# Kernel optimization log

Hardware: AMD Instinct MI355X
Metric: run time of the kernel (lower is better)

The kernel has to match this reference:

```python
import jax, jax.numpy as jnp
import numpy as np

DIM, DK, DV = 1024, 128, 128

def setup_inputs() -> dict:
    key = jax.random.key(0)
    ks = jax.random.split(key, 7)
    X = jax.random.normal(ks[0], (4, 4096, DIM), dtype=jnp.float32)
    s = DIM ** -0.5
    Wq = jax.random.normal(ks[1], (DIM, DK), dtype=jnp.float32) * s
    bq = jnp.zeros((DK,), dtype=jnp.float32)
    Wk = jax.random.normal(ks[2], (DIM, DK), dtype=jnp.float32) * s
    bk = jnp.zeros((DK,), dtype=jnp.float32)
    Wv = jax.random.normal(ks[3], (DIM, DV), dtype=jnp.float32) * s
    bv = jnp.zeros((DV,), dtype=jnp.float32)
    return {"X": X, "Wq": Wq, "bq": bq, "Wk": Wk, "bk": bk, "Wv": Wv, "bv": bv}

def reference(X, Wq, bq, Wk, bk, Wv, bv):
    scale = DK ** -0.5
    q = X @ Wq + bq              # [B, S, dk]
    k = X @ Wk + bk              # [B, S, dk]
    v = X @ Wv + bv              # [B, S, dv]
    attn = jnp.einsum('bqd,bkd->bqk', q, k) * scale  # [B, S, S]
    attn = jax.nn.softmax(attn, axis=-1)
    return jnp.einsum('bqk,bkd->bqd', attn, v)       # [B, S, dv]
```

## Files before the change

### kernel.cpp

```cpp
#include <hip/hip_runtime.h>

#define NB 4
#define SEQ 4096
#define DIMK 1024
#define DKV 128
#define SCALE 0.08838834764831845f

typedef float  f32x4  __attribute__((ext_vector_type(4)));
typedef float  f32x16 __attribute__((ext_vector_type(16)));
typedef _Float16 f16x8 __attribute__((ext_vector_type(8)));

static __device__ __forceinline__ int pkrtz(float a, float b) {
    auto h = __builtin_amdgcn_cvt_pkrtz(a, b);
    return __builtin_bit_cast(int, h);
}

static __device__ __forceinline__ void gll16(const void* g, void* l) {
    __builtin_amdgcn_global_load_lds((const __attribute__((address_space(1))) char*)g,
                                     (__attribute__((address_space(3))) char*)l, 16, 0, 0);
}

__global__ void prep_wt(const float* __restrict__ Wq, const float* __restrict__ Wk,
                        const float* __restrict__ Wv, _Float16* __restrict__ WT) {
    int tid = blockIdx.x * 256 + threadIdx.x;
    int n  = tid & 127;
    int k  = (tid >> 7) & 1023;
    int w3 = tid >> 17;
    const float* W = (w3 == 0) ? Wq : (w3 == 1) ? Wk : Wv;
    WT[((size_t)w3 * 128 + n) * 1024 + k] = (_Float16)W[(size_t)k * 128 + n];
}

__global__ __launch_bounds__(256, 2) void qkv_proj(
    const float* __restrict__ X,
    const float* __restrict__ bq, const float* __restrict__ bk, const float* __restrict__ bv,
    const _Float16* __restrict__ WT,
    _Float16* __restrict__ Qh, _Float16* __restrict__ Kh, _Float16* __restrict__ VTh) {

    __shared__ __attribute__((aligned(16))) char WTs[2][128 * 144];
    const int t = threadIdx.x;
    const int w = t >> 6, l = t & 63;
    const int lrow = l & 15, lg = l >> 4;
    const int w3   = blockIdx.x % 3;
    const int tile = blockIdx.x / 3;
    const int r0 = tile * 64;

    f32x4 acc[8] = {};
    const float* xrow = X + (size_t)(r0 + w * 16 + lrow) * DIMK;
    const _Float16* Wbase = WT + (size_t)w3 * 128 * 1024;

    const int srow = t >> 3, spart = t & 7;

    {
        int4 wreg[4];
        #pragma unroll
        for (int i = 0; i < 4; ++i)
            wreg[i] = *(const int4*)(Wbase + (size_t)(srow + 32 * i) * 1024 + spart * 8);
        #pragma unroll
        for (int i = 0; i < 4; ++i)
            *(int4*)(WTs[0] + (srow + 32 * i) * 144 + spart * 16) = wreg[i];
    }
    float4 xc0 = *(const float4*)(xrow + lg * 8);
    float4 xc1 = *(const float4*)(xrow + lg * 8 + 4);
    float4 xc2 = *(const float4*)(xrow + 32 + lg * 8);
    float4 xc3 = *(const float4*)(xrow + 32 + lg * 8 + 4);
    __syncthreads();

    for (int kt = 0; kt < 16; ++kt) {
        const int cur = kt & 1;
        const int k0n = ((kt + 1) & 15) * 64;
        float4 xn0 = *(const float4*)(xrow + k0n + lg * 8);
        float4 xn1 = *(const float4*)(xrow + k0n + lg * 8 + 4);
        float4 xn2 = *(const float4*)(xrow + k0n + 32 + lg * 8);
        float4 xn3 = *(const float4*)(xrow + k0n + 32 + lg * 8 + 4);
        int4 wreg[4];
        #pragma unroll
        for (int i = 0; i < 4; ++i)
            wreg[i] = *(const int4*)(Wbase + (size_t)(srow + 32 * i) * 1024 + k0n + spart * 8);

        #pragma unroll
        for (int kk = 0; kk < 2; ++kk) {
            f16x8 a;
            float4 u = kk ? xc2 : xc0, v = kk ? xc3 : xc1;
            a[0] = (_Float16)u.x; a[1] = (_Float16)u.y; a[2] = (_Float16)u.z; a[3] = (_Float16)u.w;
            a[4] = (_Float16)v.x; a[5] = (_Float16)v.y; a[6] = (_Float16)v.z; a[7] = (_Float16)v.w;
            #pragma unroll
            for (int n = 0; n < 8; ++n) {
                f16x8 bf = *(const f16x8*)(WTs[cur] + (n * 16 + lrow) * 144 +
                                           kk * 64 + lg * 16);
                acc[n] = __builtin_amdgcn_mfma_f32_16x16x32_f16(a, bf, acc[n], 0, 0, 0);
            }
        }
        #pragma unroll
        for (int i = 0; i < 4; ++i)
            *(int4*)(WTs[cur ^ 1] + (srow + 32 * i) * 144 + spart * 16) = wreg[i];
        __syncthreads();
        xc0 = xn0; xc1 = xn1; xc2 = xn2; xc3 = xn3;
    }

    const float* bias = (w3 == 0) ? bq : (w3 == 1) ? bk : bv;
    #pragma unroll
    for (int n = 0; n < 8; ++n) {
        int col = n * 16 + lrow;
        float bv_ = bias[col];
        #pragma unroll
        for (int j = 0; j < 4; ++j) {
            int grow = r0 + w * 16 + lg * 4 + j;
            float val = acc[n][j] + bv_;
            if (w3 == 0) {
                Qh[(size_t)grow * DKV + col] = (_Float16)(val * SCALE);
            } else if (w3 == 1) {
                Kh[(size_t)grow * DKV + col] = (_Float16)val;
            } else {
                int b = grow >> 12, sp = grow & 4095;
                VTh[((size_t)b * DKV + col) * SEQ + sp] = (_Float16)val;
            }
        }
    }
}

__global__ __launch_bounds__(256, 2) void attn_kernel(
    const _Float16* __restrict__ Qh, const _Float16* __restrict__ Kh,
    const _Float16* __restrict__ VTh, float* __restrict__ out) {

    __shared__ __attribute__((aligned(16))) char lds[65536];

    const int t = threadIdx.x;
    const int w = t >> 6, l = t & 63;
    const int lq = l & 31;
    const int hi = l >> 5;

    const int work = (blockIdx.x & 7) * 64 + (blockIdx.x >> 3);
    const int b  = work >> 7;
    const int qt = work & 127;
    const int q0 = qt * 32;

    char* Kw = lds + w * 16384;
    char* Vw = Kw + 8192;

    f16x8 qf[8];
    #pragma unroll
    for (int c = 0; c < 8; ++c)
        qf[c] = *(const f16x8*)(Qh + (size_t)(b * SEQ + q0 + lq) * DKV + c * 16 + hi * 8);

    f32x16 o[4] = {};
    float m = -INFINITY, lsum = 0.f;

    const _Float16* Kbase = Kh + (size_t)(b * SEQ + w * 1024) * DKV;
    const _Float16* Vbase = VTh + (size_t)b * DKV * SEQ + w * 1024;

    const int krow_ = l >> 4;
    const int vdv_  = l >> 2;

#define STAGE_K(KOFF) {                                                                   \
        _Pragma("unroll")                                                                 \
        for (int i = 0; i < 8; ++i) {                                                     \
            int row = 4 * i + krow_;                                                      \
            int part = (l & 15) ^ (row & 15);                                             \
            gll16(Kbase + (size_t)((KOFF) + row) * DKV + part * 8, Kw + i * 1024);        \
        }                                                                                 \
    }
#define STAGE_V(KOFF) {                                                                   \
        _Pragma("unroll")                                                                 \
        for (int i = 0; i < 8; ++i) {                                                     \
            int dv = 16 * i + vdv_;                                                       \
            int p = (l & 3) ^ ((dv >> 1) & 3);                                            \
            gll16(Vbase + (size_t)dv * SEQ + (KOFF) + p * 8, Vw + i * 1024);              \
        }                                                                                 \
    }

    STAGE_K(0)
    STAGE_V(0)

    for (int kt = 0; kt < 32; ++kt) {
        const int kn = ((kt + 1) & 31) * 32;

        asm volatile("s_waitcnt vmcnt(0)" ::: "memory");
        __builtin_amdgcn_sched_barrier(0);

        f32x16 sa = {}, sb = {};
        #pragma unroll
        for (int c = 0; c < 4; ++c) {
            f16x8 kfa = *(const f16x8*)(Kw + lq * 256 +
                                        (((2 * c + hi) * 16) ^ ((lq & 15) << 4)));
            f16x8 kfb = *(const f16x8*)(Kw + lq * 256 +
                                        (((2 * (c + 4) + hi) * 16) ^ ((lq & 15) << 4)));
            sa = __builtin_amdgcn_mfma_f32_32x32x16_f16(kfa, qf[c], sa, 0, 0, 0);
            sb = __builtin_amdgcn_mfma_f32_32x32x16_f16(kfb, qf[c + 4], sb, 0, 0, 0);
        }
        f32x16 s = sa + sb;

        asm volatile("s_waitcnt lgkmcnt(0)" ::: "memory");
        __builtin_amdgcn_sched_barrier(0);
        STAGE_K(kn)

        float red[8];
        #pragma unroll
        for (int r = 0; r < 8; ++r) red[r] = fmaxf(s[2 * r], s[2 * r + 1]);
        #pragma unroll
        for (int r = 0; r < 4; ++r) red[r] = fmaxf(red[r], red[r + 4]);
        red[0] = fmaxf(red[0], red[2]);
        red[1] = fmaxf(red[1], red[3]);
        float tm = fmaxf(red[0], red[1]);
        tm = fmaxf(tm, __shfl_xor(tm, 32));

        if (__any(tm > m + 8.f)) {
            float mnew = fmaxf(m, tm);
            float corr = __expf(m - mnew);
            m = mnew;
            lsum *= corr;
            #pragma unroll
            for (int dvt = 0; dvt < 4; ++dvt) o[dvt] *= corr;
        }
        #pragma unroll
        for (int r = 0; r < 16; ++r) s[r] = __expf(s[r] - m);
        float sr[8];
        #pragma unroll
        for (int r = 0; r < 8; ++r) sr[r] = s[2 * r] + s[2 * r + 1];
        #pragma unroll
        for (int r = 0; r < 4; ++r) sr[r] += sr[r + 4];
        sr[0] += sr[2]; sr[1] += sr[3];
        float ts = sr[0] + sr[1];
        ts += __shfl_xor(ts, 32);
        lsum += ts;

        int wv[8];
        #pragma unroll
        for (int i = 0; i < 8; ++i) wv[i] = pkrtz(s[2 * i], s[2 * i + 1]);

        #pragma unroll
        for (int s_ = 0; s_ < 2; ++s_) {
            const int base = s_ * 4;
            int x0 = __shfl_xor(wv[base + 0], 32);
            int x1 = __shfl_xor(wv[base + 1], 32);
            int x2 = __shfl_xor(wv[base + 2], 32);
            int x3 = __shfl_xor(wv[base + 3], 32);
            union { int i[4]; f16x8 v; } bu;
            bu.i[0] = hi ? x2 : wv[base + 0];
            bu.i[1] = hi ? x3 : wv[base + 1];
            bu.i[2] = hi ? wv[base + 2] : x0;
            bu.i[3] = hi ? wv[base + 3] : x1;
            #pragma unroll
            for (int dvt = 0; dvt < 4; ++dvt) {
                int rv = dvt * 32 + lq;
                f16x8 vf = *(const f16x8*)(Vw + rv * 64 +
                                           (((s_ * 2 + hi) ^ ((rv >> 1) & 3)) * 16));
                o[dvt] = __builtin_amdgcn_mfma_f32_32x32x16_f16(vf, bu.v, o[dvt], 0, 0, 0);
            }
        }

        asm volatile("s_waitcnt lgkmcnt(0)" ::: "memory");
        __builtin_amdgcn_sched_barrier(0);
        STAGE_V(kn)
    }
#undef STAGE_K
#undef STAGE_V

    float* obuf  = (float*)lds;
    float* mlbuf = (float*)(lds + 49152);

    __syncthreads();
    if (w == 1 || w == 3) {
        int sb_ = (w == 3);
        #pragma unroll
        for (int dvt = 0; dvt < 4; ++dvt)
            #pragma unroll
            for (int r = 0; r < 16; ++r)
                obuf[sb_ * 4096 + (dvt * 16 + r) * 64 + l] = o[dvt][r];
        if (l < 32) {
            mlbuf[sb_ * 64 + l * 2 + 0] = m;
            mlbuf[sb_ * 64 + l * 2 + 1] = lsum;
        }
    }
    __syncthreads();
    if (w == 0 || w == 2) {
        int sb_ = (w == 2);
        float mo  = mlbuf[sb_ * 64 + lq * 2 + 0];
        float lo_ = mlbuf[sb_ * 64 + lq * 2 + 1];
        float mn = fmaxf(m, mo);
        float ca = __expf(m - mn);
        float cb = __expf(mo - mn);
        m = mn;
        lsum = lsum * ca + lo_ * cb;
        #pragma unroll
        for (int dvt = 0; dvt < 4; ++dvt)
            #pragma unroll
            for (int r = 0; r < 16; ++r)
                o[dvt][r] = o[dvt][r] * ca + obuf[sb_ * 4096 + (dvt * 16 + r) * 64 + l] * cb;
    }
    __syncthreads();
    if (w == 2) {
        #pragma unroll
        for (int dvt = 0; dvt < 4; ++dvt)
            #pragma unroll
            for (int r = 0; r < 16; ++r)
                obuf[(dvt * 16 + r) * 64 + l] = o[dvt][r];
        if (l < 32) {
            mlbuf[l * 2 + 0] = m;
            mlbuf[l * 2 + 1] = lsum;
        }
    }
    __syncthreads();
    if (w == 0) {
        float mo  = mlbuf[lq * 2 + 0];
        float lo_ = mlbuf[lq * 2 + 1];
        float mn = fmaxf(m, mo);
        float ca = __expf(m - mn);
        float cb = __expf(mo - mn);
        float rl = 1.0f / (lsum * ca + lo_ * cb);
        #pragma unroll
        for (int dvt = 0; dvt < 4; ++dvt)
            #pragma unroll
            for (int r = 0; r < 16; ++r)
                o[dvt][r] = (o[dvt][r] * ca + obuf[(dvt * 16 + r) * 64 + l] * cb) * rl;
    }
    __syncthreads();
    float* tbuf = (float*)lds;
    if (w == 0) {
        #pragma unroll
        for (int dvt = 0; dvt < 4; ++dvt)
            #pragma unroll
            for (int r = 0; r < 16; ++r) {
                int dv = dvt * 32 + (r & 3) + 8 * (r >> 2) + 4 * hi;
                tbuf[lq * 132 + dv] = o[dvt][r];
            }
    }
    __syncthreads();
    const size_t obase = (size_t)(b * SEQ + qt * 32) * DKV;
    int row = t >> 3, c0 = (t & 7) * 16;
    #pragma unroll
    for (int i = 0; i < 4; ++i) {
        float4 v = *(const float4*)(tbuf + row * 132 + c0 + i * 4);
        *(float4*)(out + obase + row * 128 + c0 + i * 4) = v;
    }
}

extern "C" void kernel_launch(void* const* d_in, const int* in_sizes, int n_in,
                              void* d_out, int out_size, void* d_ws, size_t ws_size,
                              hipStream_t stream) {
    const float* X  = (const float*)d_in[0];
    const float* Wq = (const float*)d_in[1];
    const float* bq = (const float*)d_in[2];
    const float* Wk = (const float*)d_in[3];
    const float* bk = (const float*)d_in[4];
    const float* Wv = (const float*)d_in[5];
    const float* bv = (const float*)d_in[6];
    float* out = (float*)d_out;

    const size_t nqe = (size_t)NB * SEQ * DKV;
    _Float16* Qh  = (_Float16*)d_ws;
    _Float16* Kh  = Qh  + nqe;
    _Float16* VTh = Kh  + nqe;
    _Float16* WTh = VTh + nqe;

    prep_wt<<<(3 * 1024 * 128) / 256, 256, 0, stream>>>(Wq, Wk, Wv, WTh);
    qkv_proj<<<(NB * SEQ / 64) * 3, 256, 0, stream>>>(X, bq, bk, bv, WTh, Qh, Kh, VTh);
    attn_kernel<<<NB * 128, 256, 0, stream>>>(Qh, Kh, VTh, out);
}
```

Baseline: 118.9 us.

## Split attention keys across two blocks with combine kernel and shared K/V LDS buffer

Splits the key range into two halves when workspace allows, so the attention grid doubles from 512 to 1024 blocks. The second split writes fp16 partial outputs plus per-row max and sum, and a new combine kernel merges the two splits into the output. K and V now share one per-wave LDS buffer, halving LDS to about 33KB so more blocks fit per CU, with the K and V stages serialized inside each iteration. The qkv_proj block order is also remapped. The cost is an extra kernel, extra global traffic, fp16 rounding of half the partial outputs, and less load/compute overlap because of the shared buffer.

```diff
diff --git a/kernel.cpp b/kernel.cpp
--- a/kernel.cpp
+++ b/kernel.cpp
@@ -4,11 +4,13 @@
 #define SEQ 4096
 #define DIMK 1024
 #define DKV 128
+#define NS (NB * SEQ)
 #define SCALE 0.08838834764831845f
 
 typedef float  f32x4  __attribute__((ext_vector_type(4)));
 typedef float  f32x16 __attribute__((ext_vector_type(16)));
 typedef _Float16 f16x8 __attribute__((ext_vector_type(8)));
+typedef _Float16 f16x4 __attribute__((ext_vector_type(4)));
 
 static __device__ __forceinline__ int pkrtz(float a, float b) {
     auto h = __builtin_amdgcn_cvt_pkrtz(a, b);
@@ -40,8 +42,9 @@
     const int t = threadIdx.x;
     const int w = t >> 6, l = t & 63;
     const int lrow = l & 15, lg = l >> 4;
-    const int w3   = blockIdx.x % 3;
-    const int tile = blockIdx.x / 3;
+    const int work = (blockIdx.x & 7) * 96 + (blockIdx.x >> 3);
+    const int w3   = work % 3;
+    const int tile = work / 3;
     const int r0 = tile * 64;
 
     f32x4 acc[8] = {};
@@ -120,22 +123,26 @@
 
 __global__ __launch_bounds__(256, 2) void attn_kernel(
     const _Float16* __restrict__ Qh, const _Float16* __restrict__ Kh,
-    const _Float16* __restrict__ VTh, float* __restrict__ out) {
-
-    __shared__ __attribute__((aligned(16))) char lds[65536];
+    const _Float16* __restrict__ VTh, float* __restrict__ out,
+    _Float16* __restrict__ O1h, float* __restrict__ ml,
+    int nsplit, int kps) {
+
+    __shared__ __attribute__((aligned(16))) char lds[33280];
 
     const int t = threadIdx.x;
     const int w = t >> 6, l = t & 63;
     const int lq = l & 31;
     const int hi = l >> 5;
 
-    const int work = (blockIdx.x & 7) * 64 + (blockIdx.x >> 3);
-    const int b  = work >> 7;
+    const int cpx = gridDim.x >> 3;
+    const int work = (blockIdx.x & 7) * cpx + (blockIdx.x >> 3);
+    const int bs = work >> 7;
     const int qt = work & 127;
+    const int b  = (nsplit == 2) ? (bs >> 1) : bs;
+    const int s  = (nsplit == 2) ? (bs & 1) : 0;
     const int q0 = qt * 32;
 
-    char* Kw = lds + w * 16384;
-    char* Vw = Kw + 8192;
+    char* KVw = lds + w * 8192;
 
     f16x8 qf[8];
     #pragma unroll
@@ -145,8 +152,11 @@
     f32x16 o[4] = {};
     float m = -INFINITY, lsum = 0.f;
 
-    const _Float16* Kbase = Kh + (size_t)(b * SEQ + w * 1024) * DKV;
-    const _Float16* Vbase = VTh + (size_t)b * DKV * SEQ + w * 1024;
+    const int wkeys = kps >> 2;
+    const int kts = wkeys >> 5;
+    const int koff0 = s * kps + w * wkeys;
+    const _Float16* Kbase = Kh + (size_t)(b * SEQ + koff0) * DKV;
+    const _Float16* Vbase = VTh + (size_t)b * DKV * SEQ + koff0;
 
     const int krow_ = l >> 4;
     const int vdv_  = l >> 2;
@@ -156,7 +166,7 @@
         for (int i = 0; i < 8; ++i) {                                                     \
             int row = 4 * i + krow_;                                                      \
             int part = (l & 15) ^ (row & 15);                                             \
-            gll16(Kbase + (size_t)((KOFF) + row) * DKV + part * 8, Kw + i * 1024);        \
+            gll16(Kbase + (size_t)((KOFF) + row) * DKV + part * 8, KVw + i * 1024);       \
         }                                                                                 \
     }
 #define STAGE_V(KOFF) {                                                                   \
@@ -164,15 +174,15 @@
         for (int i = 0; i < 8; ++i) {                                                     \
             int dv = 16 * i + vdv_;                                                       \
             int p = (l & 3) ^ ((dv >> 1) & 3);                                            \
-            gll16(Vbase + (size_t)dv * SEQ + (KOFF) + p * 8, Vw + i * 1024);              \
+            gll16(Vbase + (size_t)dv * SEQ + (KOFF) + p * 8, KVw + i * 1024);             \
         }                                                                                 \
     }
 
     STAGE_K(0)
-    STAGE_V(0)
-
-    for (int kt = 0; kt < 32; ++kt) {
-        const int kn = ((kt + 1) & 31) * 32;
+
+    for (int kt = 0; kt < kts; ++kt) {
+        const int k0 = kt * 32;
+        const int knext = (kt + 1 == kts) ? 0 : (kt + 1) * 32;
 
         asm volatile("s_waitcnt vmcnt(0)" ::: "memory");
         __builtin_amdgcn_sched_barrier(0);
@@ -180,22 +190,22 @@
         f32x16 sa = {}, sb = {};
         #pragma unroll
         for (int c = 0; c < 4; ++c) {
-            f16x8 kfa = *(const f16x8*)(Kw + lq * 256 +
+            f16x8 kfa = *(const f16x8*)(KVw + lq * 256 +
                                         (((2 * c + hi) * 16) ^ ((lq & 15) << 4)));
-            f16x8 kfb = *(const f16x8*)(Kw + lq * 256 +
+            f16x8 kfb = *(const f16x8*)(KVw + lq * 256 +
                                         (((2 * (c + 4) + hi) * 16) ^ ((lq & 15) << 4)));
             sa = __builtin_amdgcn_mfma_f32_32x32x16_f16(kfa, qf[c], sa, 0, 0, 0);
             sb = __builtin_amdgcn_mfma_f32_32x32x16_f16(kfb, qf[c + 4], sb, 0, 0, 0);
         }
-        f32x16 s = sa + sb;
+        f32x16 sv = sa + sb;
 
         asm volatile("s_waitcnt lgkmcnt(0)" ::: "memory");
         __builtin_amdgcn_sched_barrier(0);
-        STAGE_K(kn)
+        STAGE_V(k0)
 
         float red[8];
         #pragma unroll
-        for (int r = 0; r < 8; ++r) red[r] = fmaxf(s[2 * r], s[2 * r + 1]);
+        for (int r = 0; r < 8; ++r) red[r] = fmaxf(sv[2 * r], sv[2 * r + 1]);
         #pragma unroll
         for (int r = 0; r < 4; ++r) red[r] = fmaxf(red[r], red[r + 4]);
         red[0] = fmaxf(red[0], red[2]);
@@ -212,10 +222,10 @@
             for (int dvt = 0; dvt < 4; ++dvt) o[dvt] *= corr;
         }
         #pragma unroll
-        for (int r = 0; r < 16; ++r) s[r] = __expf(s[r] - m);
+        for (int r = 0; r < 16; ++r) sv[r] = __expf(sv[r] - m);
         float sr[8];
         #pragma unroll
-        for (int r = 0; r < 8; ++r) sr[r] = s[2 * r] + s[2 * r + 1];
+        for (int r = 0; r < 8; ++r) sr[r] = sv[2 * r] + sv[2 * r + 1];
         #pragma unroll
         for (int r = 0; r < 4; ++r) sr[r] += sr[r + 4];
         sr[0] += sr[2]; sr[1] += sr[3];
@@ -225,7 +235,10 @@
 
         int wv[8];
         #pragma unroll
-        for (int i = 0; i < 8; ++i) wv[i] = pkrtz(s[2 * i], s[2 * i + 1]);
+        for (int i = 0; i < 8; ++i) wv[i] = pkrtz(sv[2 * i], sv[2 * i + 1]);
+
+        asm volatile("s_waitcnt vmcnt(0)" ::: "memory");
+        __builtin_amdgcn_sched_barrier(0);
 
         #pragma unroll
         for (int s_ = 0; s_ < 2; ++s_) {
@@ -242,7 +255,7 @@
             #pragma unroll
             for (int dvt = 0; dvt < 4; ++dvt) {
                 int rv = dvt * 32 + lq;
-                f16x8 vf = *(const f16x8*)(Vw + rv * 64 +
+                f16x8 vf = *(const f16x8*)(KVw + rv * 64 +
                                            (((s_ * 2 + hi) ^ ((rv >> 1) & 3)) * 16));
                 o[dvt] = __builtin_amdgcn_mfma_f32_32x32x16_f16(vf, bu.v, o[dvt], 0, 0, 0);
             }
@@ -250,14 +263,16 @@
 
         asm volatile("s_waitcnt lgkmcnt(0)" ::: "memory");
         __builtin_amdgcn_sched_barrier(0);
-        STAGE_V(kn)
+        STAGE_K(knext)
     }
 #undef STAGE_K
 #undef STAGE_V
+    asm volatile("s_waitcnt vmcnt(0)" ::: "memory");
 
     float* obuf  = (float*)lds;
-    float* mlbuf = (float*)(lds + 49152);
-
+    float* mlbuf = (float*)(lds + 32768);
+
+    float lfin = 0.f;
     __syncthreads();
     if (w == 1 || w == 3) {
         int sb_ = (w == 3);
@@ -306,12 +321,18 @@
         float mn = fmaxf(m, mo);
         float ca = __expf(m - mn);
         float cb = __expf(mo - mn);
-        float rl = 1.0f / (lsum * ca + lo_ * cb);
+        lfin = lsum * ca + lo_ * cb;
+        float rl = 1.0f / lfin;
         #pragma unroll
         for (int dvt = 0; dvt < 4; ++dvt)
             #pragma unroll
             for (int r = 0; r < 16; ++r)
                 o[dvt][r] = (o[dvt][r] * ca + obuf[(dvt * 16 + r) * 64 + l] * cb) * rl;
+        if (nsplit == 2 && l < 32) {
+            int qg = b * SEQ + qt * 32 + lq;
+            ml[(size_t)(s * 2 + 0) * NS + qg] = mn;
+            ml[(size_t)(s * 2 + 1) * NS + qg] = lfin;
+        }
     }
     __syncthreads();
     float* tbuf = (float*)lds;
@@ -327,11 +348,42 @@
     __syncthreads();
     const size_t obase = (size_t)(b * SEQ + qt * 32) * DKV;
     int row = t >> 3, c0 = (t & 7) * 16;
-    #pragma unroll
-    for (int i = 0; i < 4; ++i) {
-        float4 v = *(const float4*)(tbuf + row * 132 + c0 + i * 4);
-        *(float4*)(out + obase + row * 128 + c0 + i * 4) = v;
-    }
+    if (s == 0) {
+        #pragma unroll
+        for (int i = 0; i < 4; ++i) {
+            float4 v = *(const float4*)(tbuf + row * 132 + c0 + i * 4);
+            *(float4*)(out + obase + row * 128 + c0 + i * 4) = v;
+        }
+    } else {
+        #pragma unroll
+        for (int i = 0; i < 4; ++i) {
+            float4 v = *(const float4*)(tbuf + row * 132 + c0 + i * 4);
+            f16x4 h = {(_Float16)v.x, (_Float16)v.y, (_Float16)v.z, (_Float16)v.w};
+            *(f16x4*)(O1h + obase + row * 128 + c0 + i * 4) = h;
+        }
+    }
+}
+
+__global__ __launch_bounds__(256) void combine_kernel(
+    float* __restrict__ out, const _Float16* __restrict__ O1h,
+    const float* __restrict__ ml) {
+    int g = blockIdx.x * 256 + threadIdx.x;
+    int r = g >> 5;
+    int c0 = (g & 31) * 4;
+    float m0 = ml[r],                  l0 = ml[(size_t)NS + r];
+    float m1 = ml[(size_t)2 * NS + r], l1 = ml[(size_t)3 * NS + r];
+    float M = fmaxf(m0, m1);
+    float w0 = l0 * __expf(m0 - M);
+    float w1 = l1 * __expf(m1 - M);
+    float inv = 1.0f / (w0 + w1);
+    float4 a = *(const float4*)(out + (size_t)r * DKV + c0);
+    f16x4 h = *(const f16x4*)(O1h + (size_t)r * DKV + c0);
+    float4 res;
+    res.x = (w0 * a.x + w1 * (float)h[0]) * inv;
+    res.y = (w0 * a.y + w1 * (float)h[1]) * inv;
+    res.z = (w0 * a.z + w1 * (float)h[2]) * inv;
+    res.w = (w0 * a.w + w1 * (float)h[3]) * inv;
+    *(float4*)(out + (size_t)r * DKV + c0) = res;
 }
 
 extern "C" void kernel_launch(void* const* d_in, const int* in_sizes, int n_in,
@@ -351,8 +403,21 @@
     _Float16* Kh  = Qh  + nqe;
     _Float16* VTh = Kh  + nqe;
     _Float16* WTh = VTh + nqe;
+    size_t f16_bytes = (3 * nqe + (size_t)3 * 128 * 1024) * sizeof(_Float16);
+    f16_bytes = (f16_bytes + 255) & ~(size_t)255;
+
+    size_t o1_bytes = nqe * sizeof(_Float16);
+    size_t ml_bytes = (size_t)4 * NS * sizeof(float);
+    int nsplit = (ws_size >= f16_bytes + o1_bytes + ml_bytes) ? 2 : 1;
+    int kps = SEQ / nsplit;
+
+    _Float16* O1h = (_Float16*)((char*)d_ws + f16_bytes);
+    float* ml = (float*)((char*)d_ws + f16_bytes + o1_bytes);
 
     prep_wt<<<(3 * 1024 * 128) / 256, 256, 0, stream>>>(Wq, Wk, Wv, WTh);
     qkv_proj<<<(NB * SEQ / 64) * 3, 256, 0, stream>>>(X, bq, bk, bv, WTh, Qh, Kh, VTh);
-    attn_kernel<<<NB * 128, 256, 0, stream>>>(Qh, Kh, VTh, out);
-}
+    attn_kernel<<<NB * 128 * nsplit, 256, 0, stream>>>(Qh, Kh, VTh, out, O1h, ml,
+                                                       nsplit, kps);
+    if (nsplit == 2)
+        combine_kernel<<<(NS * 32) / 256, 256, 0, stream>>>(out, O1h, ml);
+}
```

New measurement: 122.5 us. 3.0% more time.
